# Kernel tuning notes

Hardware: AMD Instinct MI355X
Metric: run time of the kernel (lower is better)

The kernel has to match this reference:

```python
import jax, jax.numpy as jnp
import numpy as np

B, N, C = 8, 2048, 151  # batch, num rois, n_obj_classes
D_IN = C + 4            # RELPN_WITH_BBOX_INFO adds 4 normalized box coords
HID = 64


def setup_inputs() -> dict:
    key = jax.random.key(0)
    ks = jax.random.split(key, 8)
    # rois: [B, N, 5] = (batch_idx, x1, y1, x2, y2) in pixel coords
    boxes = jax.random.uniform(ks[0], (B, N, 4), dtype=jnp.float32) * 600.0
    rois = jnp.concatenate([jnp.zeros((B, N, 1), jnp.float32), boxes], axis=2)
    roi_feat = jax.random.normal(ks[1], (B, N, C), dtype=jnp.float32)
    im_info = jnp.ones((B, 3), jnp.float32) * 600.0  # (h, w, scale)
    s1 = 1.0 / np.sqrt(D_IN)
    s2 = 1.0 / np.sqrt(HID)
    return {
        "rois": rois,
        "roi_feat": roi_feat,
        "im_info": im_info,
        "w1_sub": jax.random.normal(ks[2], (D_IN, HID), jnp.float32) * s1,
        "b1_sub": jnp.zeros((HID,), jnp.float32),
        "w2_sub": jax.random.normal(ks[3], (HID, HID), jnp.float32) * s2,
        "b2_sub": jnp.zeros((HID,), jnp.float32),
        "w1_obj": jax.random.normal(ks[4], (D_IN, HID), jnp.float32) * s1,
        "b1_obj": jnp.zeros((HID,), jnp.float32),
        "w2_obj": jax.random.normal(ks[5], (HID, HID), jnp.float32) * s2,
        "b2_obj": jnp.zeros((HID,), jnp.float32),
        "K": 2048,
    }


def _mlp(x, w1, b1, w2, b2):
    return jax.nn.relu(x @ w1 + b1) @ w2 + b2


def reference(rois, roi_feat, im_info, w1_sub, b1_sub, w2_sub, b2_sub,
              w1_obj, b1_obj, w2_obj, b2_obj, K):
    b, n, _ = roi_feat.shape
    # normalized bbox info appended to roi features (RELPN_WITH_BBOX_INFO)
    xy = rois[:, :, 1:3] / im_info[:, 1][:, None, None]
    wh = rois[:, :, 3:5] / im_info[:, 0][:, None, None]
    feat = jnp.concatenate([roi_feat, xy, wh], axis=2)  # [B, N, 155]
    feat = jax.lax.stop_gradient(feat)  # original uses roi_feat4prop.detach()
    x_sub = _mlp(feat, w1_sub, b1_sub, w2_sub, b2_sub)  # [B, N, 64]
    x_obj = _mlp(feat, w1_obj, b1_obj, w2_obj, b2_obj)  # [B, N, 64]
    # bilinear pair scores: [B, N, N] -> [B, N*N]
    bil = jnp.einsum("bnd,bmd->bnm", x_sub, x_obj).reshape(b, n * n)
    vis_score = jax.nn.sigmoid(bil)  # [B, N*N]
    # proposal layer: top-K scoring (sub, obj) pairs per image
    top_scores, top_idx = jax.lax.top_k(vis_score, K)  # [B, K]
    sub_idx = top_idx // n
    obj_idx = top_idx % n
    boxes = rois[:, :, 1:5]  # [B, N, 4]
    sub_boxes = jnp.take_along_axis(boxes, sub_idx[:, :, None], axis=1)
    obj_boxes = jnp.take_along_axis(boxes, obj_idx[:, :, None], axis=1)
    roi_pairs = jnp.concatenate([sub_boxes, obj_boxes], axis=2)  # [B, K, 8]
    roi_proposals = jnp.stack([sub_idx, obj_idx], axis=2)        # [B, K, 2]
    return roi_pairs, roi_proposals, top_scores, vis_score
```

## Files before the change

### kernel.cpp

```cpp
#include <hip/hip_runtime.h>
#include <math.h>

#define NB 8
#define NN_ROI 2048
#define C_FEAT 151
#define D_IN 155
#define HID 64
#define K_TOP 2048
#define NN2 (NN_ROI*NN_ROI)
#define CAP 4096
#define NKB 1024
#define SLOTS 131072
#define LCAP 512
#define BM 128
#define BN 128
#define LSTR 132

#define WS_XS    0x0
#define WS_XO    0x400000
#define WS_CNT2  0x800000
#define WS_FLAGS 0x800040
#define WS_CAND2 0x800080
#define WS_NEED  (0x800080 + NB*SLOTS*8)

__device__ __forceinline__ float sigmoid_fast(float x) {
    return 1.0f / (1.0f + __expf(-x));
}

__global__ __launch_bounds__(256) void mlp_kernel(
    const float* __restrict__ rois, const float* __restrict__ roi_feat,
    const float* __restrict__ im_info,
    const float* __restrict__ w1_sub, const float* __restrict__ b1_sub,
    const float* __restrict__ w2_sub, const float* __restrict__ b2_sub,
    const float* __restrict__ w1_obj, const float* __restrict__ b1_obj,
    const float* __restrict__ w2_obj, const float* __restrict__ b2_obj,
    float* __restrict__ Xs, float* __restrict__ Xo)
{
    __shared__ __align__(16) float featL[64][156];
    __shared__ __align__(16) float hL[64][68];
    const int tid   = threadIdx.x;
    const int pass  = blockIdx.x >> 8;
    const int chunk = blockIdx.x & 255;
    const int row0  = chunk * 64;
    const int b     = row0 >> 11;
    const float* w1 = pass ? w1_obj : w1_sub;
    const float* w2 = pass ? w2_obj : w2_sub;
    const float* b1 = pass ? b1_obj : b1_sub;
    const float* b2 = pass ? b2_obj : b2_sub;
    float* X = pass ? Xo : Xs;
    const float im0 = im_info[b*3+0];
    const float im1 = im_info[b*3+1];

    for (int i = tid; i < 64*C_FEAT; i += 256) {
        const int r = i / C_FEAT, d = i - r*C_FEAT;
        featL[r][d] = roi_feat[(size_t)(row0+r)*C_FEAT + d];
    }
    if (tid < 64) {
        const int r = tid;
        #pragma unroll
        for (int c = 0; c < 4; ++c)
            featL[r][C_FEAT+c] = rois[(size_t)(row0+r)*5 + 1 + c] / (c < 2 ? im1 : im0);
    }
    __syncthreads();

    const int tx = tid & 15, ty = tid >> 4;
    float acc[4][4] = {};
    for (int d4 = 0; d4 < 38; ++d4) {
        const int d = d4*4;
        float wv[4][4], fv[4][4];
        #pragma unroll
        for (int q = 0; q < 4; ++q)
            *(float4*)wv[q] = *(const float4*)&w1[(d+q)*HID + tx*4];
        #pragma unroll
        for (int i = 0; i < 4; ++i)
            *(float4*)fv[i] = *(const float4*)&featL[ty*4+i][d];
        #pragma unroll
        for (int q = 0; q < 4; ++q)
            #pragma unroll
            for (int i = 0; i < 4; ++i)
                #pragma unroll
                for (int j = 0; j < 4; ++j)
                    acc[i][j] = fmaf(fv[i][q], wv[q][j], acc[i][j]);
    }
    #pragma unroll
    for (int d = 152; d < 155; ++d) {
        float wv[4];
        *(float4*)wv = *(const float4*)&w1[d*HID + tx*4];
        #pragma unroll
        for (int i = 0; i < 4; ++i) {
            const float f = featL[ty*4+i][d];
            #pragma unroll
            for (int j = 0; j < 4; ++j)
                acc[i][j] = fmaf(f, wv[j], acc[i][j]);
        }
    }
    {
        float b1v[4];
        *(float4*)b1v = *(const float4*)&b1[tx*4];
        #pragma unroll
        for (int i = 0; i < 4; ++i)
            #pragma unroll
            for (int j = 0; j < 4; ++j) {
                const float v = acc[i][j] + b1v[j];
                hL[ty*4+i][tx*4+j] = v > 0.0f ? v : 0.0f;
            }
    }
    __syncthreads();

    float x[4][4] = {};
    for (int k4 = 0; k4 < 16; ++k4) {
        const int k = k4*4;
        float wv[4][4], hv[4][4];
        #pragma unroll
        for (int q = 0; q < 4; ++q)
            *(float4*)wv[q] = *(const float4*)&w2[(k+q)*HID + tx*4];
        #pragma unroll
        for (int i = 0; i < 4; ++i)
            *(float4*)hv[i] = *(const float4*)&hL[ty*4+i][k];
        #pragma unroll
        for (int q = 0; q < 4; ++q)
            #pragma unroll
            for (int i = 0; i < 4; ++i)
                #pragma unroll
                for (int j = 0; j < 4; ++j)
                    x[i][j] = fmaf(hv[i][q], wv[q][j], x[i][j]);
    }
    {
        float b2v[4];
        *(float4*)b2v = *(const float4*)&b2[tx*4];
        #pragma unroll
        for (int i = 0; i < 4; ++i) {
            *(float4*)&X[(size_t)(row0 + ty*4 + i)*HID + tx*4] = make_float4(
                x[i][0]+b2v[0], x[i][1]+b2v[1], x[i][2]+b2v[2], x[i][3]+b2v[3]);
        }
    }
}

__global__ __launch_bounds__(256) void bil_kernel(
    const float* __restrict__ Xs, const float* __restrict__ Xo,
    float* __restrict__ vis, int* __restrict__ cnt2, int2* __restrict__ cand2,
    int* __restrict__ flags)
{
    __shared__ __align__(16) float As[32][LSTR];
    __shared__ __align__(16) float Bs[32][LSTR];
    __shared__ int2 lcand[LCAP];
    __shared__ int lcnt, lbase;
    const int tid = threadIdx.x;
    const int tx = tid & 15, ty = tid >> 4;
    const int bm = blockIdx.x * BM, bn = blockIdx.y * BN, b = blockIdx.z;
    if (tid == 0) lcnt = 0;

    const float4* Ag = (const float4*)(Xs + ((size_t)b*NN_ROI + bm)*HID);
    const float4* Bg = (const float4*)(Xo + ((size_t)b*NN_ROI + bn)*HID);

    float acc[8][8];
    #pragma unroll
    for (int i = 0; i < 8; ++i)
        #pragma unroll
        for (int j = 0; j < 8; ++j) acc[i][j] = 0.0f;

    for (int kh = 0; kh < 2; ++kh) {
        __syncthreads();
        #pragma unroll
        for (int i = 0; i < 4; ++i) {
            const int lin = i*256 + tid;
            const int r = lin >> 3, k4 = lin & 7;
            const float4 va = Ag[r*16 + kh*8 + k4];
            As[k4*4+0][r] = va.x; As[k4*4+1][r] = va.y;
            As[k4*4+2][r] = va.z; As[k4*4+3][r] = va.w;
            const float4 vb = Bg[r*16 + kh*8 + k4];
            Bs[k4*4+0][r] = vb.x; Bs[k4*4+1][r] = vb.y;
            Bs[k4*4+2][r] = vb.z; Bs[k4*4+3][r] = vb.w;
        }
        __syncthreads();
        #pragma unroll 8
        for (int k = 0; k < 32; ++k) {
            const float4 a0 = *(const float4*)&As[k][ty*8];
            const float4 a1 = *(const float4*)&As[k][ty*8+4];
            const float4 b0 = *(const float4*)&Bs[k][tx*4];
            const float4 b1 = *(const float4*)&Bs[k][64+tx*4];
            const float a[8] = {a0.x,a0.y,a0.z,a0.w,a1.x,a1.y,a1.z,a1.w};
            const float bb[8] = {b0.x,b0.y,b0.z,b0.w,b1.x,b1.y,b1.z,b1.w};
            #pragma unroll
            for (int i = 0; i < 8; ++i)
                #pragma unroll
                for (int j = 0; j < 8; ++j)
                    acc[i][j] = fmaf(a[i], bb[j], acc[i][j]);
        }
    }

    const size_t visbase = (size_t)b * NN2;
    #pragma unroll
    for (int i = 0; i < 8; ++i) {
        const int row = bm + ty*8 + i;
        float f[8];
        #pragma unroll
        for (int j = 0; j < 8; ++j) {
            const float s = sigmoid_fast(acc[i][j]);
            f[j] = s;
            const int ku = 0x3F800000 - __float_as_int(s);
            if (ku < NKB) {
                const int col = bn + (j < 4 ? tx*4 + j : 64 + tx*4 + (j-4));
                const int idx = row*NN_ROI + col;
                const int p = atomicAdd(&lcnt, 1);
                if (p < LCAP) lcand[p] = make_int2(idx, __float_as_int(s));
                else {
                    const int gp = atomicAdd(&cnt2[b], 1);
                    if (gp < SLOTS) cand2[(size_t)b*SLOTS + gp] =
                        make_int2(idx, __float_as_int(s));
                }
            }
        }
        *(float4*)&vis[visbase + (size_t)row*NN_ROI + bn + tx*4] =
            make_float4(f[0], f[1], f[2], f[3]);
        *(float4*)&vis[visbase + (size_t)row*NN_ROI + bn + 64 + tx*4] =
            make_float4(f[4], f[5], f[6], f[7]);
    }
    __syncthreads();
    int n = lcnt; if (n > LCAP) n = LCAP;
    if (tid == 0) lbase = atomicAdd(&cnt2[b], n);
    __syncthreads();
    const int bs = lbase;
    for (int i = tid; i < n; i += 256) {
        const int p = bs + i;
        if (p < SLOTS) cand2[(size_t)b*SLOTS + p] = lcand[i];
    }
}

__global__ __launch_bounds__(1024) void topk_kernel(
    const int* __restrict__ cnt2, const int2* __restrict__ cand2,
    const float* __restrict__ rois,
    float* __restrict__ pairs, float* __restrict__ props, float* __restrict__ scores,
    int* __restrict__ flags)
{
    __shared__ float kv[CAP];
    __shared__ int   ki[CAP];
    __shared__ int   hist[NKB];
    __shared__ int   part[64];
    __shared__ int   scnt;
    __shared__ float sthr;
    const int b = blockIdx.x, tid = threadIdx.x;
    int M = cnt2[b]; if (M > SLOTS) M = SLOTS;
    if (cnt2[b] > SLOTS) atomicOr(flags, 4);

    for (int i = tid; i < NKB; i += 1024) hist[i] = 0;
    if (tid == 0) scnt = 0;
    __syncthreads();
    for (int i = tid; i < M; i += 1024) {
        const int k = 0x3F800000 - cand2[(size_t)b*SLOTS + i].y;
        atomicAdd(&hist[k], 1);
    }
    __syncthreads();
    if (tid < 64) {
        int s = 0;
        for (int i = 0; i < 16; ++i) s += hist[tid*16 + i];
        part[tid] = s;
    }
    __syncthreads();
    if (tid == 0) {
        int cum = 0, kT = NKB - 1; bool found = false;
        for (int c = 0; c < 64; ++c) {
            if (cum + part[c] >= K_TOP) {
                for (int i = c*16; i < c*16 + 16; ++i) {
                    cum += hist[i];
                    if (cum >= K_TOP) { kT = i; found = true; break; }
                }
                break;
            }
            cum += part[c];
        }
        if (!found) atomicOr(flags, 16);
        sthr = __int_as_float(0x3F800000 - kT);
    }
    __syncthreads();
    const float th = sthr;
    for (int c = tid; c < CAP; c += 1024) { kv[c] = -1.0e30f; ki[c] = 0x7FFFFFFF; }
    __syncthreads();
    for (int i = tid; i < M; i += 1024) {
        const int2 e = cand2[(size_t)b*SLOTS + i];
        const float s = __int_as_float(e.y);
        if (s >= th) {
            const int p = atomicAdd(&scnt, 1);
            if (p < CAP) { kv[p] = s; ki[p] = e.x; }
        }
    }
    __syncthreads();
    if (tid == 0) {
        if (scnt < K_TOP) atomicOr(flags, 2);
        if (scnt > CAP)   atomicOr(flags, 4);
    }
    for (int kk = 2; kk <= CAP; kk <<= 1)
        for (int j = kk >> 1; j > 0; j >>= 1) {
            for (int t = tid; t < CAP/2; t += 1024) {
                const int i = 2*t - (t & (j-1));
                const int p = i + j;
                const bool dir = (i & kk) == 0;
                const float vi = kv[i], vp = kv[p];
                const int ii = ki[i], ip = ki[p];
                const bool ge = (vi > vp) || (vi == vp && ii <= ip);
                if (dir ? !ge : ge) { kv[i]=vp; kv[p]=vi; ki[i]=ip; ki[p]=ii; }
            }
            __syncthreads();
        }
    for (int k = tid; k < K_TOP-1; k += 1024) {
        const bool okp = (kv[k] > kv[k+1]) || (kv[k] == kv[k+1] && ki[k] <= ki[k+1]);
        if (!okp) atomicOr(flags, 8);
    }
    for (int k = tid; k < K_TOP; k += 1024) {
        const float v = kv[k]; const int idx = ki[k];
        int sub = 0, obj = 0; float sc = 0.f;
        float4 sb = make_float4(0,0,0,0), ob = make_float4(0,0,0,0);
        if (idx != 0x7FFFFFFF) {
            sub = idx >> 11; obj = idx & (NN_ROI-1);
            sc = v;
            const float* rs = rois + ((size_t)b*NN_ROI + sub)*5 + 1;
            const float* ro = rois + ((size_t)b*NN_ROI + obj)*5 + 1;
            sb = make_float4(rs[0],rs[1],rs[2],rs[3]);
            ob = make_float4(ro[0],ro[1],ro[2],ro[3]);
        }
        const size_t o = (size_t)b*K_TOP + k;
        *(float4*)&pairs[o*8]   = sb;
        *(float4*)&pairs[o*8+4] = ob;
        props[o*2]   = (float)sub;
        props[o*2+1] = (float)obj;
        scores[o]    = sc;
    }
}

__global__ void check_kernel(const int* __restrict__ flags, float* __restrict__ pairs)
{
    const int f = *flags;
    if (f) pairs[0] = 1e5f * (float)f;
}

__global__ void sentinel_kernel(float* out) { out[0] = 1e5f; }

extern "C" void kernel_launch(void* const* d_in, const int* in_sizes, int n_in,
                              void* d_out, int out_size, void* d_ws, size_t ws_size,
                              hipStream_t stream)
{
    static const int EXP_SIZES[12] = {81920, 2473984, 24, 9920, 64, 4096, 64,
                                      9920, 64, 4096, 64, 1};
    bool ok = (n_in == 12) && (out_size == 33734656) && (ws_size >= (size_t)WS_NEED);
    if (ok) for (int i = 0; i < 12; ++i) if (in_sizes[i] != EXP_SIZES[i]) { ok = false; break; }
    if (!ok) { sentinel_kernel<<<1, 1, 0, stream>>>((float*)d_out); return; }

    const float* rois     = (const float*)d_in[0];
    const float* roi_feat = (const float*)d_in[1];
    const float* im_info  = (const float*)d_in[2];
    const float* w1_sub   = (const float*)d_in[3];
    const float* b1_sub   = (const float*)d_in[4];
    const float* w2_sub   = (const float*)d_in[5];
    const float* b2_sub   = (const float*)d_in[6];
    const float* w1_obj   = (const float*)d_in[7];
    const float* b1_obj   = (const float*)d_in[8];
    const float* w2_obj   = (const float*)d_in[9];
    const float* b2_obj   = (const float*)d_in[10];

    char* ws = (char*)d_ws;
    float* Xs   = (float*)(ws + WS_XS);
    float* Xo   = (float*)(ws + WS_XO);
    int* cnt2   = (int*)  (ws + WS_CNT2);
    int* flags  = (int*)  (ws + WS_FLAGS);
    int2* cand2 = (int2*) (ws + WS_CAND2);

    float* out    = (float*)d_out;
    float* pairs  = out;
    float* props  = out + 131072;
    float* scores = out + 163840;
    float* vis    = out + 180224;

    hipMemsetAsync(ws + WS_CNT2, 0, 0x80, stream);
    mlp_kernel<<<512, 256, 0, stream>>>(rois, roi_feat, im_info,
        w1_sub, b1_sub, w2_sub, b2_sub, w1_obj, b1_obj, w2_obj, b2_obj, Xs, Xo);
    bil_kernel<<<dim3(16,16,NB), 256, 0, stream>>>(Xs, Xo, vis, cnt2, cand2, flags);
    topk_kernel<<<NB, 1024, 0, stream>>>(cnt2, cand2, rois, pairs, props, scores, flags);
    check_kernel<<<1, 1, 0, stream>>>(flags, pairs);
}
```

Baseline: 171.3 us.

## Widen bilinear tile to 128x256 with XOR-swizzled shared memory

Each block of the bilinear kernel now covers 256 output columns instead of 128, so every thread accumulates an 8x16 register tile and the grid has half as many blocks. The padded shared-memory layout is replaced by an XOR swizzle to avoid bank conflicts, and launch bounds request 3 blocks per multiprocessor. The aim is more FMA work per shared-memory load and less redundant loading of A. The cost is higher register pressure (128 accumulators), a larger shared footprint and fewer blocks to spread across CUs. The vis store stays vectorized and the local candidate capacity shrinks to fit.

After: 488.8 us. 185% more time.

```diff
diff --git a/kernel.cpp b/kernel.cpp
--- a/kernel.cpp
+++ b/kernel.cpp
@@ -11,10 +11,9 @@
 #define CAP 4096
 #define NKB 1024
 #define SLOTS 131072
-#define LCAP 512
+#define LCAP 448
 #define BM 128
-#define BN 128
-#define LSTR 132
+#define BN 256
 
 #define WS_XS    0x0
 #define WS_XO    0x400000
@@ -136,13 +135,13 @@
     }
 }
 
-__global__ __launch_bounds__(256) void bil_kernel(
+__global__ __launch_bounds__(256, 3) void bil_kernel(
     const float* __restrict__ Xs, const float* __restrict__ Xo,
     float* __restrict__ vis, int* __restrict__ cnt2, int2* __restrict__ cand2,
     int* __restrict__ flags)
 {
-    __shared__ __align__(16) float As[32][LSTR];
-    __shared__ __align__(16) float Bs[32][LSTR];
+    __shared__ __align__(16) float As[32][128];
+    __shared__ __align__(16) float Bs[32][256];
     __shared__ int2 lcand[LCAP];
     __shared__ int lcnt, lbase;
     const int tid = threadIdx.x;
@@ -153,38 +152,49 @@
     const float4* Ag = (const float4*)(Xs + ((size_t)b*NN_ROI + bm)*HID);
     const float4* Bg = (const float4*)(Xo + ((size_t)b*NN_ROI + bn)*HID);
 
-    float acc[8][8];
+    float acc[8][16];
     #pragma unroll
     for (int i = 0; i < 8; ++i)
         #pragma unroll
-        for (int j = 0; j < 8; ++j) acc[i][j] = 0.0f;
+        for (int j = 0; j < 16; ++j) acc[i][j] = 0.0f;
 
     for (int kh = 0; kh < 2; ++kh) {
+        if (kh) __syncthreads();
+        #pragma unroll
+        for (int it = 0; it < 4; ++it) {
+            const int lin = it*256 + tid;
+            const int r = lin >> 3, k4 = lin & 7;
+            const float4 v = Ag[r*16 + kh*8 + k4];
+            const int rs = r ^ ((k4 & 3) << 3);
+            As[k4*4+0][rs] = v.x; As[k4*4+1][rs] = v.y;
+            As[k4*4+2][rs] = v.z; As[k4*4+3][rs] = v.w;
+        }
+        #pragma unroll
+        for (int it = 0; it < 8; ++it) {
+            const int lin = it*256 + tid;
+            const int r = lin >> 3, k4 = lin & 7;
+            const float4 v = Bg[r*16 + kh*8 + k4];
+            const int rs = r ^ ((k4 & 3) << 3);
+            Bs[k4*4+0][rs] = v.x; Bs[k4*4+1][rs] = v.y;
+            Bs[k4*4+2][rs] = v.z; Bs[k4*4+3][rs] = v.w;
+        }
         __syncthreads();
-        #pragma unroll
-        for (int i = 0; i < 4; ++i) {
-            const int lin = i*256 + tid;
-            const int r = lin >> 3, k4 = lin & 7;
-            const float4 va = Ag[r*16 + kh*8 + k4];
-            As[k4*4+0][r] = va.x; As[k4*4+1][r] = va.y;
-            As[k4*4+2][r] = va.z; As[k4*4+3][r] = va.w;
-            const float4 vb = Bg[r*16 + kh*8 + k4];
-            Bs[k4*4+0][r] = vb.x; Bs[k4*4+1][r] = vb.y;
-            Bs[k4*4+2][r] = vb.z; Bs[k4*4+3][r] = vb.w;
-        }
-        __syncthreads();
-        #pragma unroll 8
+        #pragma unroll 4
         for (int k = 0; k < 32; ++k) {
-            const float4 a0 = *(const float4*)&As[k][ty*8];
-            const float4 a1 = *(const float4*)&As[k][ty*8+4];
-            const float4 b0 = *(const float4*)&Bs[k][tx*4];
-            const float4 b1 = *(const float4*)&Bs[k][64+tx*4];
+            const int swz = ((k >> 2) & 3) << 3;
+            const int am = (ty*8) ^ swz;
+            const float4 a0 = *(const float4*)&As[k][am];
+            const float4 a1 = *(const float4*)&As[k][am + 4];
+            float bb[16];
+            *(float4*)&bb[0]  = *(const float4*)&Bs[k][(tx*4) ^ swz];
+            *(float4*)&bb[4]  = *(const float4*)&Bs[k][(64  + tx*4) ^ swz];
+            *(float4*)&bb[8]  = *(const float4*)&Bs[k][(128 + tx*4) ^ swz];
+            *(float4*)&bb[12] = *(const float4*)&Bs[k][(192 + tx*4) ^ swz];
             const float a[8] = {a0.x,a0.y,a0.z,a0.w,a1.x,a1.y,a1.z,a1.w};
-            const float bb[8] = {b0.x,b0.y,b0.z,b0.w,b1.x,b1.y,b1.z,b1.w};
             #pragma unroll
             for (int i = 0; i < 8; ++i)
                 #pragma unroll
-                for (int j = 0; j < 8; ++j)
+                for (int j = 0; j < 16; ++j)
                     acc[i][j] = fmaf(a[i], bb[j], acc[i][j]);
         }
     }
@@ -193,14 +203,14 @@
     #pragma unroll
     for (int i = 0; i < 8; ++i) {
         const int row = bm + ty*8 + i;
-        float f[8];
-        #pragma unroll
-        for (int j = 0; j < 8; ++j) {
+        float f[16];
+        #pragma unroll
+        for (int j = 0; j < 16; ++j) {
             const float s = sigmoid_fast(acc[i][j]);
             f[j] = s;
             const int ku = 0x3F800000 - __float_as_int(s);
             if (ku < NKB) {
-                const int col = bn + (j < 4 ? tx*4 + j : 64 + tx*4 + (j-4));
+                const int col = bn + (j >> 2)*64 + tx*4 + (j & 3);
                 const int idx = row*NN_ROI + col;
                 const int p = atomicAdd(&lcnt, 1);
                 if (p < LCAP) lcand[p] = make_int2(idx, __float_as_int(s));
@@ -211,10 +221,10 @@
                 }
             }
         }
-        *(float4*)&vis[visbase + (size_t)row*NN_ROI + bn + tx*4] =
-            make_float4(f[0], f[1], f[2], f[3]);
-        *(float4*)&vis[visbase + (size_t)row*NN_ROI + bn + 64 + tx*4] =
-            make_float4(f[4], f[5], f[6], f[7]);
+        #pragma unroll
+        for (int q = 0; q < 4; ++q)
+            *(float4*)&vis[visbase + (size_t)row*NN_ROI + bn + q*64 + tx*4] =
+                make_float4(f[q*4+0], f[q*4+1], f[q*4+2], f[q*4+3]);
     }
     __syncthreads();
     int n = lcnt; if (n > LCAP) n = LCAP;
@@ -373,7 +383,7 @@
     hipMemsetAsync(ws + WS_CNT2, 0, 0x80, stream);
     mlp_kernel<<<512, 256, 0, stream>>>(rois, roi_feat, im_info,
         w1_sub, b1_sub, w2_sub, b2_sub, w1_obj, b1_obj, w2_obj, b2_obj, Xs, Xo);
-    bil_kernel<<<dim3(16,16,NB), 256, 0, stream>>>(Xs, Xo, vis, cnt2, cand2, flags);
+    bil_kernel<<<dim3(16, 8, NB), 256, 0, stream>>>(Xs, Xo, vis, cnt2, cand2, flags);
     topk_kernel<<<NB, 1024, 0, stream>>>(cnt2, cand2, rois, pairs, props, scores, flags);
     check_kernel<<<1, 1, 0, stream>>>(flags, pairs);
 }
```
